# Performance work log

Measured on AMD Instinct MI355X. Metric: run time of the kernel, lower is better.

## Reference

```python
import jax, jax.numpy as jnp
import numpy as np

# Involution2D config (matches init_kwargs)
F = 256          # filters
K = 3            # kernel_size
G = 16           # groups
RR = 4           # reduce_ratio
BN_EPS = 1e-3    # keras BatchNormalization default epsilon


def setup_inputs() -> dict:
    key = jax.random.key(0)
    ks = jax.random.split(key, 8)
    C = 256
    Cr = F // RR                    # reduce_mapping channels = 64
    KKG = K * K * G                 # span_mapping channels = 144
    s = lambda k, sh, fan: jax.random.normal(k, sh, jnp.float32) * (1.0 / np.sqrt(fan))
    return {
        "x": jax.random.normal(ks[0], (4, 128, 128, C), jnp.float32),
        # reduce_mapping: 1x1 conv + BN(inference) + relu
        "Wr": s(ks[1], (C, Cr), C),
        "br": jnp.zeros((Cr,), jnp.float32),
        "gamma": jnp.ones((Cr,), jnp.float32),
        "beta": jnp.zeros((Cr,), jnp.float32),
        "mean": jax.random.normal(ks[2], (Cr,), jnp.float32) * 0.1,
        "var": jax.random.uniform(ks[3], (Cr,), jnp.float32, 0.5, 1.5),
        # span_mapping: 1x1 conv -> K*K*G dynamic weights
        "Ws": s(ks[4], (Cr, KKG), Cr),
        "bs": jnp.zeros((KKG,), jnp.float32),
        # initial_mapping: 1x1 conv -> F (applied since F != K*K*G)
        "Wi": s(ks[5], (C, F), C),
        "bi": jnp.zeros((F,), jnp.float32),
    }


def reference(x, Wr, br, gamma, beta, mean, var, Ws, bs, Wi, bi):
    B, H, W, _ = x.shape
    KK = K * K
    # reduce_mapping: 1x1 conv + BN(inference) + relu
    r = jnp.einsum('bhwc,cd->bhwd', x, Wr) + br
    r = jax.nn.relu((r - mean) * jax.lax.rsqrt(var + BN_EPS) * gamma + beta)
    # span_mapping: per-pixel dynamic kernel weights [B,H,W,KK*G] -> [B,H,W,G,1,KK]
    w = jnp.einsum('bhwd,dk->bhwk', r, Ws) + bs
    w = w.reshape(B, H, W, G, KK)[:, :, :, :, None, :]
    # initial_mapping: 1x1 conv -> F channels
    xi = jnp.einsum('bhwc,cf->bhwf', x, Wi) + bi
    # tf.image.extract_patches (SAME, stride=1, rate=1): layout is
    # (kernel_pos major, channel minor), i.e. flat index = kpos*F + c
    pad = (K - 1) // 2
    xp = jnp.pad(xi, ((0, 0), (pad, pad), (pad, pad), (0, 0)))
    patches = jnp.stack(
        [xp[:, i:i + H, j:j + W, :] for i in range(K) for j in range(K)],
        axis=3)                                   # [B,H,W,KK,F]
    # faithful to the original K.reshape of the flat [KK*F] axis
    patches = patches.reshape(B, H, W, G, F // G, KK)
    out = jnp.sum(w * patches, axis=-1)           # [B,H,W,G,F//G]
    return out.reshape(B, H, W, F)
```

## Files before the change

kernel.cpp:

```cpp
#include <hip/hip_runtime.h>

#define BN_EPS 1e-3f

typedef __attribute__((ext_vector_type(8))) short bf16x8;
typedef __attribute__((ext_vector_type(4))) float f32x4;

__device__ inline unsigned short f2b(float f) {
    unsigned int u = __float_as_uint(f);
    unsigned int r = (u + 0x7fffu + ((u >> 16) & 1u)) >> 16;
    return (unsigned short)r;
}
__device__ inline float b2f(unsigned short h) {
    return __uint_as_float(((unsigned int)h) << 16);
}

__global__ void k_prep(const float* __restrict__ Wi, const float* __restrict__ Wr,
                       const float* __restrict__ Ws,
                       unsigned short* __restrict__ Bt, unsigned short* __restrict__ Wst) {
    int t = blockIdx.x * 256 + threadIdx.x;
    if (t < 320 * 256) {
        int n = t >> 8, k = t & 255;
        float v = (n < 256) ? Wi[k * 256 + n] : Wr[k * 64 + (n - 256)];
        Bt[t] = f2b(v);
    } else {
        int t2 = t - 320 * 256;
        if (t2 < 144 * 64) {
            int n = t2 >> 6, k = t2 & 63;
            Wst[t2] = f2b(Ws[k * 144 + n]);
        }
    }
}

#define AXIP 264
#define ASMN (128 * AXIP)
#define ARSP 72

__global__ __launch_bounds__(512, 4) void k_xiw(
    const float* __restrict__ x, const unsigned short* __restrict__ Bt,
    const unsigned short* __restrict__ Wst,
    const float* __restrict__ bi, const float* __restrict__ br,
    const float* __restrict__ gamma, const float* __restrict__ beta,
    const float* __restrict__ mean, const float* __restrict__ var,
    const float* __restrict__ bs,
    unsigned short* __restrict__ xi_g, unsigned short* __restrict__ w_g)
{
    __shared__ __attribute__((aligned(16))) unsigned short sm[ASMN];
    const int tid = threadIdx.x;
    const long long px0 = (long long)blockIdx.x * 128;

    const int wv = tid >> 6;
    const int lane = tid & 63;
    const int col = lane & 15;
    const int quad = lane >> 4;
    const int mh = wv >> 2;
    const int nq = wv & 3;

#pragma unroll
    for (int it = 0; it < 8; ++it) {
        const int flat = it * 512 + tid;
        const int px = flat >> 5;
        const int cho = (flat & 31) * 8;
        const float* src = x + (px0 + px) * 256 + cho;
        float4 v0 = *(const float4*)&src[0];
        float4 v1 = *(const float4*)&src[4];
        int4 pk;
        pk.x = (int)((unsigned)f2b(v0.x) | ((unsigned)f2b(v0.y) << 16));
        pk.y = (int)((unsigned)f2b(v0.z) | ((unsigned)f2b(v0.w) << 16));
        pk.z = (int)((unsigned)f2b(v1.x) | ((unsigned)f2b(v1.y) << 16));
        pk.w = (int)((unsigned)f2b(v1.z) | ((unsigned)f2b(v1.w) << 16));
        *(int4*)&sm[px * AXIP + cho] = pk;
    }
    __syncthreads();

    f32x4 acc[5][4];
#pragma unroll
    for (int jj = 0; jj < 5; ++jj)
#pragma unroll
        for (int m = 0; m < 4; ++m) acc[jj][m] = (f32x4){0.f, 0.f, 0.f, 0.f};

#pragma unroll
    for (int kc = 0; kc < 8; ++kc) {
        const int kb = kc * 32 + quad * 8;
        bf16x8 a[4];
#pragma unroll
        for (int m = 0; m < 4; ++m)
            a[m] = *(const bf16x8*)&sm[(mh * 64 + m * 16 + col) * AXIP + kb];
#pragma unroll
        for (int jj = 0; jj < 5; ++jj) {
            const int j = nq * 5 + jj;
            bf16x8 b = *(const bf16x8*)&Bt[(j * 16 + col) * 256 + kb];
#pragma unroll
            for (int m = 0; m < 4; ++m)
                acc[jj][m] = __builtin_amdgcn_mfma_f32_16x16x32_bf16(a[m], b, acc[jj][m], 0, 0, 0);
        }
    }
    __syncthreads();

#pragma unroll
    for (int jj = 0; jj < 5; ++jj) {
        const int j = nq * 5 + jj;
        if (j < 16) {
            const int n = j * 16 + col;
            const float bv = bi[n];
#pragma unroll
            for (int m = 0; m < 4; ++m) {
                const long long pxb = px0 + mh * 64 + m * 16 + quad * 4;
#pragma unroll
                for (int rg = 0; rg < 4; ++rg)
                    xi_g[(pxb + rg) * 256 + n] = f2b(acc[jj][m][rg] + bv);
            }
        } else {
            const int d = (j - 16) * 16 + col;
            const float sc = gamma[d] * rsqrtf(var[d] + BN_EPS);
            const float bb2 = (br[d] - mean[d]) * sc + beta[d];
#pragma unroll
            for (int m = 0; m < 4; ++m) {
                const int rowb = mh * 64 + m * 16 + quad * 4;
#pragma unroll
                for (int rg = 0; rg < 4; ++rg) {
                    const float v = acc[jj][m][rg] * sc + bb2;
                    sm[(rowb + rg) * ARSP + d] = f2b(fmaxf(v, 0.f));
                }
            }
        }
    }
    __syncthreads();

    f32x4 wa[9];
#pragma unroll
    for (int j = 0; j < 9; ++j) wa[j] = (f32x4){0.f, 0.f, 0.f, 0.f};
#pragma unroll
    for (int kc = 0; kc < 2; ++kc) {
        const int kb = kc * 32 + quad * 8;
        bf16x8 ra = *(const bf16x8*)&sm[(wv * 16 + col) * ARSP + kb];
#pragma unroll
        for (int j = 0; j < 9; ++j) {
            bf16x8 wb = *(const bf16x8*)&Wst[(j * 16 + col) * 64 + kb];
            wa[j] = __builtin_amdgcn_mfma_f32_16x16x32_bf16(ra, wb, wa[j], 0, 0, 0);
        }
    }
#pragma unroll
    for (int j = 0; j < 9; ++j) {
        const int n = j * 16 + col;
        const float bv = bs[n];
        const long long pxb = px0 + wv * 16 + quad * 4;
#pragma unroll
        for (int rg = 0; rg < 4; ++rg)
            w_g[(pxb + rg) * 144 + n] = f2b(wa[j][rg] + bv);
    }
}

#define GXIP 264
#define GWL_OFF (100 * GXIP)
#define GSMN (GWL_OFF + 64 * 144)

__global__ __launch_bounds__(512, 4) void k_gather(
    const unsigned short* __restrict__ xi_g, const unsigned short* __restrict__ w_g,
    float* __restrict__ out)
{
    __shared__ __attribute__((aligned(16))) unsigned short sm[GSMN];
    const int tid = threadIdx.x;
    const int b = blockIdx.x;
    const int bx = (b & 7) * 128 + (b >> 3);
    const int w0 = (bx & 15) * 8;
    const int h0 = ((bx >> 4) & 15) * 8;
    const int bb = bx >> 8;

#pragma unroll
    for (int it = 0; it < 7; ++it) {
        const int flat = it * 512 + tid;
        if (flat < 3200) {
            const int px = flat >> 5;
            const int cho = (flat & 31) * 8;
            const int hr = px / 10, hc = px - hr * 10;
            const int gh = h0 - 1 + hr, gw = w0 - 1 + hc;
            int4 v;
            if (((unsigned)gh < 128u) && ((unsigned)gw < 128u)) {
                const long long pxg = ((long long)(bb * 128 + gh)) * 128 + gw;
                v = *(const int4*)&xi_g[pxg * 256 + cho];
            } else {
                v = (int4){0, 0, 0, 0};
            }
            *(int4*)&sm[px * GXIP + cho] = v;
        }
    }
#pragma unroll
    for (int it = 0; it < 3; ++it) {
        const int flat = it * 512 + tid;
        if (flat < 1152) {
            const int px = flat / 18;
            const int cho = (flat - px * 18) * 8;
            const long long pxg =
                ((long long)(bb * 128 + h0 + (px >> 3))) * 128 + (w0 + (px & 7));
            int4 v = *(const int4*)&w_g[pxg * 144 + cho];
            *(int4*)&sm[GWL_OFF + px * 144 + cho] = v;
        }
    }
    __syncthreads();

    {
        const int g = tid & 15;
        const int pb = tid >> 4;

        const int idx0 = g * 144;
        const int kp0  = idx0 >> 8;
        const int c0   = idx0 & 255;
        int len1 = 256 - c0; if (len1 > 144) len1 = 144;
        const int kp1  = kp0 + 1;
        const int koff0 = (kp0 / 3) * 10 + (kp0 % 3);
        const int koff1 = (kp1 <= 8) ? ((kp1 / 3) * 10 + (kp1 % 3)) : 0;

#pragma unroll
        for (int jj = 0; jj < 2; ++jj) {
            const int p = pb + 32 * jj;
            const int phb = (p >> 3) * 10 + (p & 7);
            const int base0 = (phb + koff0) * GXIP + c0;
            const int base1 = (phb + koff1) * GXIP;

            float wf[9];
#pragma unroll
            for (int kk = 0; kk < 9; ++kk)
                wf[kk] = b2f(sm[GWL_OFF + p * 144 + g * 9 + kk]);

            float res[16];
            {
                int4 xv[9];
#pragma unroll
                for (int i = 0; i < 9; ++i) {
                    const int e = i * 8;
                    const int addr = (e < len1) ? (base0 + e) : (base1 + (e - len1));
                    xv[i] = *(const int4*)&sm[addr];
                }
#pragma unroll
                for (int f2 = 0; f2 < 8; ++f2) {
                    float a = 0.f;
#pragma unroll
                    for (int kk = 0; kk < 9; ++kk) {
                        const int e = f2 * 9 + kk;
                        const int word = ((const int*)&xv[e >> 3])[(e >> 1) & 3];
                        const unsigned short u = (e & 1) ? (unsigned short)(((unsigned)word) >> 16)
                                                         : (unsigned short)(word & 0xffff);
                        a += wf[kk] * b2f(u);
                    }
                    res[f2] = a;
                }
            }
            {
                int4 xv[9];
#pragma unroll
                for (int i = 9; i < 18; ++i) {
                    const int e = i * 8;
                    const int addr = (e < len1) ? (base0 + e) : (base1 + (e - len1));
                    xv[i - 9] = *(const int4*)&sm[addr];
                }
#pragma unroll
                for (int f2 = 8; f2 < 16; ++f2) {
                    float a = 0.f;
#pragma unroll
                    for (int kk = 0; kk < 9; ++kk) {
                        const int e = f2 * 9 + kk;
                        const int i = (e >> 3) - 9;
                        const int word = ((const int*)&xv[i])[(e >> 1) & 3];
                        const unsigned short u = (e & 1) ? (unsigned short)(((unsigned)word) >> 16)
                                                         : (unsigned short)(word & 0xffff);
                        a += wf[kk] * b2f(u);
                    }
                    res[f2] = a;
                }
            }

            const long long orow =
                (((long long)(bb * 128 + h0 + (p >> 3))) * 128 + (w0 + (p & 7))) * 256 + g * 16;
#pragma unroll
            for (int q = 0; q < 4; ++q) {
                float4 o = {res[q * 4 + 0], res[q * 4 + 1], res[q * 4 + 2], res[q * 4 + 3]};
                *(float4*)&out[orow + q * 4] = o;
            }
        }
    }
}

extern "C" void kernel_launch(void* const* d_in, const int* in_sizes, int n_in,
                              void* d_out, int out_size, void* d_ws, size_t ws_size,
                              hipStream_t stream) {
    const float* x     = (const float*)d_in[0];
    const float* Wr    = (const float*)d_in[1];
    const float* br    = (const float*)d_in[2];
    const float* gamma = (const float*)d_in[3];
    const float* beta  = (const float*)d_in[4];
    const float* mean  = (const float*)d_in[5];
    const float* var   = (const float*)d_in[6];
    const float* Ws    = (const float*)d_in[7];
    const float* bs    = (const float*)d_in[8];
    const float* Wi    = (const float*)d_in[9];
    const float* bi    = (const float*)d_in[10];
    float* out = (float*)d_out;

    unsigned char* ws = (unsigned char*)d_ws;
    unsigned short* Bt   = (unsigned short*)(ws + 0);
    unsigned short* Wst  = (unsigned short*)(ws + 163840);
    unsigned short* xi_g = (unsigned short*)(ws + 182272);
    unsigned short* w_g  = (unsigned short*)(ws + 33736704);

    k_prep<<<dim3(356), dim3(256), 0, stream>>>(Wi, Wr, Ws, Bt, Wst);
    k_xiw<<<dim3(512), dim3(512), 0, stream>>>(
        x, Bt, Wst, bi, br, gamma, beta, mean, var, bs, xi_g, w_g);
    k_gather<<<dim3(1024), dim3(512), 0, stream>>>(xi_g, w_g, out);
}
```

Before: 198.1 us.

## Halve pixels per block in xi/w GEMM kernel and remap waves to tiles

```diff
diff --git a/kernel.cpp b/kernel.cpp
--- a/kernel.cpp
+++ b/kernel.cpp
@@ -32,8 +32,9 @@
 }
 
 #define AXIP 264
-#define ASMN (128 * AXIP)
+#define ARS_OFF (64 * AXIP)
 #define ARSP 72
+#define ASMN (ARS_OFF + 64 * ARSP)
 
 __global__ __launch_bounds__(512, 4) void k_xiw(
     const float* __restrict__ x, const unsigned short* __restrict__ Bt,
@@ -46,17 +47,15 @@
 {
     __shared__ __attribute__((aligned(16))) unsigned short sm[ASMN];
     const int tid = threadIdx.x;
-    const long long px0 = (long long)blockIdx.x * 128;
+    const long long px0 = (long long)blockIdx.x * 64;
 
     const int wv = tid >> 6;
     const int lane = tid & 63;
     const int col = lane & 15;
     const int quad = lane >> 4;
-    const int mh = wv >> 2;
-    const int nq = wv & 3;
-
-#pragma unroll
-    for (int it = 0; it < 8; ++it) {
+
+#pragma unroll
+    for (int it = 0; it < 4; ++it) {
         const int flat = it * 512 + tid;
         const int px = flat >> 5;
         const int cho = (flat & 31) * 8;
@@ -72,81 +71,108 @@
     }
     __syncthreads();
 
-    f32x4 acc[5][4];
-#pragma unroll
-    for (int jj = 0; jj < 5; ++jj)
-#pragma unroll
-        for (int m = 0; m < 4; ++m) acc[jj][m] = (f32x4){0.f, 0.f, 0.f, 0.f};
+    f32x4 acc1[4], acc2[4], accr[4];
+#pragma unroll
+    for (int m = 0; m < 4; ++m) {
+        acc1[m] = (f32x4){0.f, 0.f, 0.f, 0.f};
+        acc2[m] = acc1[m];
+        accr[m] = acc1[m];
+    }
+
+    const unsigned short* pB1 = &Bt[(wv * 16 + col) * 256];
+    const unsigned short* pB2 = &Bt[((wv + 8) * 16 + col) * 256];
+    const unsigned short* pBr = &Bt[(256 + (wv & 3) * 16 + col) * 256];
 
 #pragma unroll
     for (int kc = 0; kc < 8; ++kc) {
         const int kb = kc * 32 + quad * 8;
-        bf16x8 a[4];
-#pragma unroll
-        for (int m = 0; m < 4; ++m)
-            a[m] = *(const bf16x8*)&sm[(mh * 64 + m * 16 + col) * AXIP + kb];
-#pragma unroll
-        for (int jj = 0; jj < 5; ++jj) {
-            const int j = nq * 5 + jj;
-            bf16x8 b = *(const bf16x8*)&Bt[(j * 16 + col) * 256 + kb];
-#pragma unroll
-            for (int m = 0; m < 4; ++m)
-                acc[jj][m] = __builtin_amdgcn_mfma_f32_16x16x32_bf16(a[m], b, acc[jj][m], 0, 0, 0);
-        }
-    }
-    __syncthreads();
-
-#pragma unroll
-    for (int jj = 0; jj < 5; ++jj) {
-        const int j = nq * 5 + jj;
-        if (j < 16) {
-            const int n = j * 16 + col;
-            const float bv = bi[n];
-#pragma unroll
-            for (int m = 0; m < 4; ++m) {
-                const long long pxb = px0 + mh * 64 + m * 16 + quad * 4;
-#pragma unroll
-                for (int rg = 0; rg < 4; ++rg)
-                    xi_g[(pxb + rg) * 256 + n] = f2b(acc[jj][m][rg] + bv);
-            }
-        } else {
-            const int d = (j - 16) * 16 + col;
+        bf16x8 a0 = *(const bf16x8*)&sm[(0 * 16 + col) * AXIP + kb];
+        bf16x8 a1 = *(const bf16x8*)&sm[(1 * 16 + col) * AXIP + kb];
+        bf16x8 a2 = *(const bf16x8*)&sm[(2 * 16 + col) * AXIP + kb];
+        bf16x8 a3 = *(const bf16x8*)&sm[(3 * 16 + col) * AXIP + kb];
+        bf16x8 b1 = *(const bf16x8*)&pB1[kb];
+        bf16x8 b2 = *(const bf16x8*)&pB2[kb];
+        acc1[0] = __builtin_amdgcn_mfma_f32_16x16x32_bf16(a0, b1, acc1[0], 0, 0, 0);
+        acc1[1] = __builtin_amdgcn_mfma_f32_16x16x32_bf16(a1, b1, acc1[1], 0, 0, 0);
+        acc1[2] = __builtin_amdgcn_mfma_f32_16x16x32_bf16(a2, b1, acc1[2], 0, 0, 0);
+        acc1[3] = __builtin_amdgcn_mfma_f32_16x16x32_bf16(a3, b1, acc1[3], 0, 0, 0);
+        acc2[0] = __builtin_amdgcn_mfma_f32_16x16x32_bf16(a0, b2, acc2[0], 0, 0, 0);
+        acc2[1] = __builtin_amdgcn_mfma_f32_16x16x32_bf16(a1, b2, acc2[1], 0, 0, 0);
+        acc2[2] = __builtin_amdgcn_mfma_f32_16x16x32_bf16(a2, b2, acc2[2], 0, 0, 0);
+        acc2[3] = __builtin_amdgcn_mfma_f32_16x16x32_bf16(a3, b2, acc2[3], 0, 0, 0);
+        if (wv < 4) {
+            bf16x8 br_ = *(const bf16x8*)&pBr[kb];
+            accr[0] = __builtin_amdgcn_mfma_f32_16x16x32_bf16(a0, br_, accr[0], 0, 0, 0);
+            accr[1] = __builtin_amdgcn_mfma_f32_16x16x32_bf16(a1, br_, accr[1], 0, 0, 0);
+            accr[2] = __builtin_amdgcn_mfma_f32_16x16x32_bf16(a2, br_, accr[2], 0, 0, 0);
+            accr[3] = __builtin_amdgcn_mfma_f32_16x16x32_bf16(a3, br_, accr[3], 0, 0, 0);
+        }
+    }
+
+    {
+        const int n1 = wv * 16 + col;
+        const int n2 = n1 + 128;
+        const float bv1 = bi[n1];
+        const float bv2 = bi[n2];
+#pragma unroll
+        for (int m = 0; m < 4; ++m) {
+            const long long pxb = px0 + m * 16 + quad * 4;
+#pragma unroll
+            for (int rg = 0; rg < 4; ++rg) {
+                xi_g[(pxb + rg) * 256 + n1] = f2b(acc1[m][rg] + bv1);
+                xi_g[(pxb + rg) * 256 + n2] = f2b(acc2[m][rg] + bv2);
+            }
+        }
+        if (wv < 4) {
+            const int d = (wv & 3) * 16 + col;
             const float sc = gamma[d] * rsqrtf(var[d] + BN_EPS);
             const float bb2 = (br[d] - mean[d]) * sc + beta[d];
 #pragma unroll
             for (int m = 0; m < 4; ++m) {
-                const int rowb = mh * 64 + m * 16 + quad * 4;
+                const int rowb = m * 16 + quad * 4;
 #pragma unroll
                 for (int rg = 0; rg < 4; ++rg) {
-                    const float v = acc[jj][m][rg] * sc + bb2;
-                    sm[(rowb + rg) * ARSP + d] = f2b(fmaxf(v, 0.f));
+                    const float v = accr[m][rg] * sc + bb2;
+                    sm[ARS_OFF + (rowb + rg) * ARSP + d] = f2b(fmaxf(v, 0.f));
                 }
             }
         }
     }
     __syncthreads();
 
-    f32x4 wa[9];
-#pragma unroll
-    for (int j = 0; j < 9; ++j) wa[j] = (f32x4){0.f, 0.f, 0.f, 0.f};
-#pragma unroll
-    for (int kc = 0; kc < 2; ++kc) {
-        const int kb = kc * 32 + quad * 8;
-        bf16x8 ra = *(const bf16x8*)&sm[(wv * 16 + col) * ARSP + kb];
-#pragma unroll
-        for (int j = 0; j < 9; ++j) {
-            bf16x8 wb = *(const bf16x8*)&Wst[(j * 16 + col) * 64 + kb];
-            wa[j] = __builtin_amdgcn_mfma_f32_16x16x32_bf16(ra, wb, wa[j], 0, 0, 0);
-        }
-    }
-#pragma unroll
-    for (int j = 0; j < 9; ++j) {
-        const int n = j * 16 + col;
-        const float bv = bs[n];
-        const long long pxb = px0 + wv * 16 + quad * 4;
-#pragma unroll
-        for (int rg = 0; rg < 4; ++rg)
-            w_g[(pxb + rg) * 144 + n] = f2b(wa[j][rg] + bv);
+    {
+        const int mt = wv & 3;
+        const int jh = wv >> 2;
+        const int jb = jh * 5;
+        const int njt = 5 - jh;
+        const int arow = ARS_OFF + (mt * 16 + col) * ARSP;
+        bf16x8 ra0 = *(const bf16x8*)&sm[arow + quad * 8];
+        bf16x8 ra1 = *(const bf16x8*)&sm[arow + 32 + quad * 8];
+
+        f32x4 wacc[5];
+#pragma unroll
+        for (int jj = 0; jj < 5; ++jj) wacc[jj] = (f32x4){0.f, 0.f, 0.f, 0.f};
+#pragma unroll
+        for (int jj = 0; jj < 5; ++jj) {
+            if (jj < njt) {
+                const unsigned short* wp = &Wst[((jb + jj) * 16 + col) * 64];
+                bf16x8 wb0 = *(const bf16x8*)&wp[quad * 8];
+                bf16x8 wb1 = *(const bf16x8*)&wp[32 + quad * 8];
+                wacc[jj] = __builtin_amdgcn_mfma_f32_16x16x32_bf16(ra0, wb0, wacc[jj], 0, 0, 0);
+                wacc[jj] = __builtin_amdgcn_mfma_f32_16x16x32_bf16(ra1, wb1, wacc[jj], 0, 0, 0);
+            }
+        }
+#pragma unroll
+        for (int jj = 0; jj < 5; ++jj) {
+            if (jj < njt) {
+                const int n = (jb + jj) * 16 + col;
+                const float bv = bs[n];
+                const long long pxb = px0 + mt * 16 + quad * 4;
+#pragma unroll
+                for (int rg = 0; rg < 4; ++rg)
+                    w_g[(pxb + rg) * 144 + n] = f2b(wacc[jj][rg] + bv);
+            }
+        }
     }
 }
 
@@ -303,7 +329,7 @@
     unsigned short* w_g  = (unsigned short*)(ws + 33736704);
 
     k_prep<<<dim3(356), dim3(256), 0, stream>>>(Wi, Wr, Ws, Bt, Wst);
-    k_xiw<<<dim3(512), dim3(512), 0, stream>>>(
+    k_xiw<<<dim3(1024), dim3(512), 0, stream>>>(
         x, Bt, Wst, bi, br, gamma, beta, mean, var, bs, xi_g, w_g);
     k_gather<<<dim3(1024), dim3(512), 0, stream>>>(xi_g, w_g, out);
 }
```

Result: faster. 188.1 us (-5.0%).
